# Kernel optimization log

Measured on AMD Instinct MI355X. Metric: run time of the kernel, lower is better.

Reference implementation:

```python
import jax, jax.numpy as jnp
import numpy as np

BLANK = 0
ALPHA = 0.25
GAMMA = 2.0
NEG = -1e30  # log-domain 'minus infinity' (finite to stay autodiff/bf16 safe)


def setup_inputs() -> dict:
    key = jax.random.key(0)
    k1, k2, k3 = jax.random.split(key, 3)
    B, T, C, S = 32, 512, 4000, 40
    tokens_btc = jax.random.normal(k1, (B, T, C), dtype=jnp.float32)
    targets_bxt = jax.random.randint(k2, (B, S), 1, C)            # labels exclude blank=0
    targets_lengths_bx1 = jax.random.randint(k3, (B,), 10, S + 1)  # per-sample target lengths
    return {
        "tokens_btc": tokens_btc,
        "targets_bxt": targets_bxt,
        "targets_lengths_bx1": targets_lengths_bx1,
    }


def _ctc_loss(log_probs_tbc, targets, target_lengths, blank):
    """Log-domain CTC forward (alpha) recursion; input lengths == T for all samples.
    Returns per-sample negative log likelihood, shape [B]."""
    T, B, C = log_probs_tbc.shape
    S = targets.shape[1]
    L = 2 * S + 1  # extended target: blank-interleaved
    ext = jnp.full((B, L), blank, dtype=targets.dtype).at[:, 1::2].set(targets)
    # skip transition (s-2 -> s) allowed iff ext[s] != blank and ext[s] != ext[s-2]
    same_as_2back = jnp.concatenate(
        [jnp.ones((B, 2), bool), ext[:, 2:] == ext[:, :-2]], axis=1)
    skip_ok = (ext != blank) & (~same_as_2back)  # [B, L]

    b_idx = jnp.arange(B)[:, None]
    lp_ext = log_probs_tbc[:, b_idx, ext]  # [T, B, L] gathered emission log-probs

    alpha0 = jnp.full((B, L), NEG, log_probs_tbc.dtype)
    alpha0 = alpha0.at[:, 0].set(lp_ext[0, :, 0]).at[:, 1].set(lp_ext[0, :, 1])

    pad1 = jnp.full((B, 1), NEG, log_probs_tbc.dtype)
    pad2 = jnp.full((B, 2), NEG, log_probs_tbc.dtype)

    def step(alpha, lp_t):
        s1 = jnp.concatenate([pad1, alpha[:, :-1]], axis=1)
        s2 = jnp.concatenate([pad2, alpha[:, :-2]], axis=1)
        a = jnp.logaddexp(alpha, s1)
        a = jnp.where(skip_ok, jnp.logaddexp(a, s2), a)
        return a + lp_t, None

    alphaT, _ = jax.lax.scan(step, alpha0, lp_ext[1:])
    end = 2 * target_lengths  # index of final blank in extended sequence
    a_last = jnp.take_along_axis(alphaT, end[:, None], axis=1)[:, 0]
    a_prev = jnp.take_along_axis(alphaT, (end - 1)[:, None], axis=1)[:, 0]
    loss = -jnp.logaddexp(a_last, a_prev)
    # zero_infinity=True: clamp infinite losses to 0
    return jnp.where(loss < 1e29, loss, 0.0)


def reference(tokens_btc, targets_bxt, targets_lengths_bx1):
    # [B,T,C] -> [T,B,C], log_softmax over classes
    log_probs_tbc = jax.nn.log_softmax(tokens_btc, axis=-1).swapaxes(0, 1)
    loss = _ctc_loss(log_probs_tbc, targets_bxt, targets_lengths_bx1, BLANK)
    # focal reweighting (alpha>0 and gamma>=0 -> enabled)
    pt = jnp.exp(-loss)
    loss = ALPHA * (1.0 - pt) ** GAMMA * loss
    return jnp.mean(loss)
```

## Files before the change

kernel.cpp:

```cpp
#include <hip/hip_runtime.h>


constexpr int B = 32;
constexpr int T = 512;
constexpr int C = 4000;
constexpr int S = 40;
constexpr int L = 2 * S + 1;
constexpr int LPS = 82;
constexpr int PF = 8;

#define NEGV -1e30f

__device__ __forceinline__ float lae(float a, float b) {
    float m = fmaxf(a, b);
    float d = fabsf(a - b);
    return m + __logf(1.0f + __expf(-d));
}

__device__ __forceinline__ float shr1_fill_neg(float x) {
    return __int_as_float(__builtin_amdgcn_update_dpp(
        __float_as_int(NEGV), __float_as_int(x),
        0x138 , 0xF, 0xF, false));
}

__global__ __launch_bounds__(256) void lse_gather_kernel(
        const float* __restrict__ tok,
        const int*   __restrict__ tgt,
        float*       __restrict__ lp) {
    const int wave = threadIdx.x >> 6, lane = threadIdx.x & 63;
    const int row  = blockIdx.x * 4 + wave;
    const int b    = row >> 9;
    const size_t row_off = (size_t)row * C;
    const float4* row4 = (const float4*)(tok + row_off);

    float s = 0.0f;
    #pragma unroll
    for (int k = 0; k < 16; ++k) {
        const int i = lane + 64 * k;
        if (i < C / 4) {
            float4 v = row4[i];
            s += __expf(v.x) + __expf(v.y) + __expf(v.z) + __expf(v.w);
        }
    }
    #pragma unroll
    for (int off = 32; off; off >>= 1) s += __shfl_xor(s, off);
    const float lse = __logf(s);

    float* dst = lp + (size_t)row * LPS;
    {
        const int l = lane;
        int lab = 0;
        if (l & 1) lab = tgt[b * S + (l >> 1)];
        dst[l] = tok[row_off + lab] - lse;
    }
    if (lane < LPS - 64) {
        const int l = 64 + lane;
        float v = 0.0f;
        if (l < L) {
            int lab = 0;
            if (l & 1) lab = tgt[b * S + (l >> 1)];
            v = tok[row_off + lab] - lse;
        }
        dst[l] = v;
    }
}

__global__ __launch_bounds__(64) void ctc_alpha_kernel(
        const float* __restrict__ lp,
        const int*   __restrict__ tgt,
        const int*   __restrict__ lens,
        float*       __restrict__ loss_b)
{
    const int b = blockIdx.x;
    const int lane = threadIdx.x;
    const int ii = (lane < 41) ? lane : 40;

    const float2* base2 = (const float2*)(lp + (size_t)b * T * LPS);

    int ti = tgt[b * S + ((ii < 39) ? ii : 39)];
    int tp = __shfl_up(ti, 1);
    const bool skip1 = (lane >= 1) && (lane <= 39) && (ti != tp);

    float2 v0 = base2[ii];
    float a0 = (lane == 0) ? v0.x : NEGV;
    float a1 = (lane == 0) ? v0.y : NEGV;

    float2 buf[PF];
    #pragma unroll
    for (int k = 0; k < PF; ++k) buf[k] = base2[(size_t)(1 + k) * 41 + ii];

    auto step = [&](float2 v) {
        float p1 = shr1_fill_neg(a1);
        float m0 = fmaxf(a0, p1);
        float n0 = m0 + __logf(__expf(a0 - m0) + __expf(p1 - m0));
        float q  = skip1 ? p1 : NEGV;
        float m1 = fmaxf(fmaxf(a1, a0), q);
        float n1 = m1 + __logf(__expf(a1 - m1) + __expf(a0 - m1) + __expf(q - m1));
        a0 = n0 + v.x;
        a1 = n1 + v.y;
    };

    int t = 1;
    for (; t + (PF - 1) < T; t += PF) {
        #pragma unroll
        for (int k = 0; k < PF; ++k) {
            float2 v = buf[k];
            buf[k] = base2[(size_t)(t + PF + k) * 41 + ii];
            step(v);
        }
    }
    #pragma unroll
    for (int k = 0; k < PF; ++k) {
        if (t + k < T) step(buf[k]);
    }

    const int len = lens[b];
    float ae = __shfl(a0, len);
    float ap = __shfl(a1, len - 1);
    if (lane == 0) {
        float loss = -lae(ae, ap);
        if (!(loss < 1e29f)) loss = 0.0f;
        float pt = __expf(-loss);
        float om = 1.0f - pt;
        loss_b[b] = 0.25f * om * om * loss;
    }
}

__global__ __launch_bounds__(64) void reduce_mean_kernel(
        const float* __restrict__ loss_b, float* __restrict__ out) {
    const int lane = threadIdx.x;
    float v = (lane < B) ? loss_b[lane] : 0.0f;
    #pragma unroll
    for (int off = 32; off; off >>= 1) v += __shfl_down(v, off);
    if (lane == 0) out[0] = v * (1.0f / B);
}

extern "C" void kernel_launch(void* const* d_in, const int* in_sizes, int n_in,
                              void* d_out, int out_size, void* d_ws, size_t ws_size,
                              hipStream_t stream) {
    const float* tok  = (const float*)d_in[0];
    const int*   tgt  = (const int*)d_in[1];
    const int*   lens = (const int*)d_in[2];
    float* out = (float*)d_out;

    float* lp     = (float*)d_ws;
    float* loss_b = lp + (size_t)B * T * LPS + 1024;

    lse_gather_kernel<<<B * T / 4, 256, 0, stream>>>(tok, tgt, lp);
    ctc_alpha_kernel<<<B, 64, 0, stream>>>(lp, tgt, lens, loss_b);
    reduce_mean_kernel<<<1, 64, 0, stream>>>(loss_b, out);
}
```

Baseline: 424.3 us.

## Fuse LSE gather and CTC alpha recursion with per-row flags to overlap stages

Merges the log-softmax gather, the CTC alpha recursion and the mean reduction into one persistent kernel. Gather blocks process rows in time-major order and set a per-row ready flag, while 8 extra blocks run the per-sample alpha recursion, spinning on 8-row flag chunks so the sequential recursion overlaps the bandwidth-bound gather. The final mean is done by the last finishing wave through an atomic counter, which removes two kernel launches. The risk is deadlock if the consumer blocks are resident while gather blocks cannot be scheduled, plus extra cost from flag polling and atomic stores.

After: 407.4 us. -4.0%, faster.

```diff
diff --git a/kernel.cpp b/kernel.cpp
--- a/kernel.cpp
+++ b/kernel.cpp
@@ -7,7 +7,10 @@
 constexpr int S = 40;
 constexpr int L = 2 * S + 1;
 constexpr int LPS = 82;
-constexpr int PF = 8;
+
+constexpr int GATHER_BLOCKS = 1016;
+constexpr int GW = GATHER_BLOCKS * 4;
+constexpr int NBLK = GATHER_BLOCKS + 8;
 
 #define NEGV -1e30f
 
@@ -23,72 +26,83 @@
         0x138 , 0xF, 0xF, false));
 }
 
-__global__ __launch_bounds__(256) void lse_gather_kernel(
+__global__ __launch_bounds__(256) void zero_flags_kernel(unsigned int* p, int n) {
+    const int i = blockIdx.x * 256 + threadIdx.x;
+    if (i < n) p[i] = 0u;
+}
+
+__global__ __launch_bounds__(256, 4) void fused_kernel(
         const float* __restrict__ tok,
         const int*   __restrict__ tgt,
-        float*       __restrict__ lp) {
+        const int*   __restrict__ lens,
+        float*       __restrict__ lp,
+        unsigned char* __restrict__ flags,
+        unsigned int* __restrict__ ctr,
+        float*       __restrict__ loss_b,
+        float*       __restrict__ out) {
     const int wave = threadIdx.x >> 6, lane = threadIdx.x & 63;
-    const int row  = blockIdx.x * 4 + wave;
-    const int b    = row >> 9;
-    const size_t row_off = (size_t)row * C;
-    const float4* row4 = (const float4*)(tok + row_off);
-
-    float s = 0.0f;
-    #pragma unroll
-    for (int k = 0; k < 16; ++k) {
-        const int i = lane + 64 * k;
-        if (i < C / 4) {
-            float4 v = row4[i];
-            s += __expf(v.x) + __expf(v.y) + __expf(v.z) + __expf(v.w);
+
+    if (blockIdx.x < GATHER_BLOCKS) {
+        const int wg = blockIdx.x * 4 + wave;
+        for (int rp = wg; rp < B * T; rp += GW) {
+            const int t  = rp >> 5;
+            const int bb = rp & 31;
+            const int row = (bb << 9) + t;
+            const size_t row_off = (size_t)row * C;
+            const float4* row4 = (const float4*)(tok + row_off);
+
+            float s = 0.0f;
+            #pragma unroll
+            for (int k = 0; k < 16; ++k) {
+                const int i = lane + 64 * k;
+                if (i < C / 4) {
+                    float4 v = row4[i];
+                    s += __expf(v.x) + __expf(v.y) + __expf(v.z) + __expf(v.w);
+                }
+            }
+            #pragma unroll
+            for (int off = 32; off; off >>= 1) s += __shfl_xor(s, off);
+            const float lse = __logf(s);
+
+            float* dst = lp + (size_t)row * LPS;
+            {
+                const int l = lane;
+                int lab = 0;
+                if (l & 1) lab = tgt[bb * S + (l >> 1)];
+                __hip_atomic_store(dst + l, tok[row_off + lab] - lse,
+                                   __ATOMIC_RELAXED, __HIP_MEMORY_SCOPE_AGENT);
+            }
+            if (lane < LPS - 64) {
+                const int l = 64 + lane;
+                float v = 0.0f;
+                if (l < L) {
+                    int lab = 0;
+                    if (l & 1) lab = tgt[bb * S + (l >> 1)];
+                    v = tok[row_off + lab] - lse;
+                }
+                __hip_atomic_store(dst + l, v,
+                                   __ATOMIC_RELAXED, __HIP_MEMORY_SCOPE_AGENT);
+            }
+            asm volatile("s_waitcnt vmcnt(0)" ::: "memory");
+            if (lane == 0)
+                __hip_atomic_store(flags + row, (unsigned char)1,
+                                   __ATOMIC_RELAXED, __HIP_MEMORY_SCOPE_AGENT);
         }
-    }
-    #pragma unroll
-    for (int off = 32; off; off >>= 1) s += __shfl_xor(s, off);
-    const float lse = __logf(s);
-
-    float* dst = lp + (size_t)row * LPS;
-    {
-        const int l = lane;
-        int lab = 0;
-        if (l & 1) lab = tgt[b * S + (l >> 1)];
-        dst[l] = tok[row_off + lab] - lse;
-    }
-    if (lane < LPS - 64) {
-        const int l = 64 + lane;
-        float v = 0.0f;
-        if (l < L) {
-            int lab = 0;
-            if (l & 1) lab = tgt[b * S + (l >> 1)];
-            v = tok[row_off + lab] - lse;
-        }
-        dst[l] = v;
-    }
-}
-
-__global__ __launch_bounds__(64) void ctc_alpha_kernel(
-        const float* __restrict__ lp,
-        const int*   __restrict__ tgt,
-        const int*   __restrict__ lens,
-        float*       __restrict__ loss_b)
-{
-    const int b = blockIdx.x;
-    const int lane = threadIdx.x;
+        return;
+    }
+
+    const int b  = ((blockIdx.x - GATHER_BLOCKS) << 2) + wave;
     const int ii = (lane < 41) ? lane : 40;
-
     const float2* base2 = (const float2*)(lp + (size_t)b * T * LPS);
+    unsigned long long* fw = (unsigned long long*)(flags + ((size_t)b << 9));
+    const unsigned long long ONESW = 0x0101010101010101ull;
 
     int ti = tgt[b * S + ((ii < 39) ? ii : 39)];
     int tp = __shfl_up(ti, 1);
     const bool skip1 = (lane >= 1) && (lane <= 39) && (ti != tp);
-
-    float2 v0 = base2[ii];
-    float a0 = (lane == 0) ? v0.x : NEGV;
-    float a1 = (lane == 0) ? v0.y : NEGV;
-
-    float2 buf[PF];
-    #pragma unroll
-    for (int k = 0; k < PF; ++k) buf[k] = base2[(size_t)(1 + k) * 41 + ii];
-
+    const int len = lens[b];
+
+    float a0, a1;
     auto step = [&](float2 v) {
         float p1 = shr1_fill_neg(a1);
         float m0 = fmaxf(a0, p1);
@@ -100,21 +114,47 @@
         a1 = n1 + v.y;
     };
 
-    int t = 1;
-    for (; t + (PF - 1) < T; t += PF) {
-        #pragma unroll
-        for (int k = 0; k < PF; ++k) {
-            float2 v = buf[k];
-            buf[k] = base2[(size_t)(t + PF + k) * 41 + ii];
-            step(v);
-        }
+    float2 bufA[8], bufB[8];
+    unsigned long long pf = 0;
+
+#define SPINCHUNK(c) do {                                                     \
+        while (pf != ONESW)                                                   \
+            pf = __hip_atomic_load(&fw[(c)], __ATOMIC_RELAXED,                \
+                                   __HIP_MEMORY_SCOPE_AGENT);                 \
+        __builtin_amdgcn_fence(__ATOMIC_ACQUIRE, "agent");                    \
+    } while (0)
+#define PREFETCHF(c) pf = ((c) < 64)                                          \
+        ? __hip_atomic_load(&fw[(c)], __ATOMIC_RELAXED,                       \
+                            __HIP_MEMORY_SCOPE_AGENT)                         \
+        : ONESW
+#define LOADCHUNK(buf, c) do { const int _t0 = (c) << 3;                      \
+        _Pragma("unroll")                                                     \
+        for (int _k = 0; _k < 8; ++_k)                                        \
+            buf[_k] = base2[(size_t)(_t0 + _k) * 41 + ii];                    \
+    } while (0)
+#define STEP8(buf) do { _Pragma("unroll")                                     \
+        for (int _k = 0; _k < 8; ++_k) step(buf[_k]); } while (0)
+
+    SPINCHUNK(0); LOADCHUNK(bufA, 0);
+    pf = 0; SPINCHUNK(1); LOADCHUNK(bufB, 1);
+    PREFETCHF(2);
+
+    {
+        float2 v0 = bufA[0];
+        a0 = (lane == 0) ? v0.x : NEGV;
+        a1 = (lane == 0) ? v0.y : NEGV;
     }
     #pragma unroll
-    for (int k = 0; k < PF; ++k) {
-        if (t + k < T) step(buf[k]);
-    }
-
-    const int len = lens[b];
+    for (int k = 1; k < 8; ++k) step(bufA[k]);
+
+    for (int c = 1; c < 63; c += 2) {
+        SPINCHUNK(c + 1); LOADCHUNK(bufA, c + 1); PREFETCHF(c + 2);
+        STEP8(bufB);
+        SPINCHUNK(c + 2); LOADCHUNK(bufB, c + 2); PREFETCHF(c + 3);
+        STEP8(bufA);
+    }
+    STEP8(bufB);
+
     float ae = __shfl(a0, len);
     float ap = __shfl(a1, len - 1);
     if (lane == 0) {
@@ -122,17 +162,26 @@
         if (!(loss < 1e29f)) loss = 0.0f;
         float pt = __expf(-loss);
         float om = 1.0f - pt;
-        loss_b[b] = 0.25f * om * om * loss;
-    }
-}
-
-__global__ __launch_bounds__(64) void reduce_mean_kernel(
-        const float* __restrict__ loss_b, float* __restrict__ out) {
-    const int lane = threadIdx.x;
-    float v = (lane < B) ? loss_b[lane] : 0.0f;
-    #pragma unroll
-    for (int off = 32; off; off >>= 1) v += __shfl_down(v, off);
-    if (lane == 0) out[0] = v * (1.0f / B);
+        __hip_atomic_store(loss_b + b, 0.25f * om * om * loss,
+                           __ATOMIC_RELAXED, __HIP_MEMORY_SCOPE_AGENT);
+    }
+    asm volatile("s_waitcnt vmcnt(0)" ::: "memory");
+    unsigned int old = 0;
+    if (lane == 0)
+        old = __hip_atomic_fetch_add(ctr, 1u, __ATOMIC_RELAXED,
+                                     __HIP_MEMORY_SCOPE_AGENT);
+    old = (unsigned int)__shfl((int)old, 0);
+    if (old == B - 1) {
+        __builtin_amdgcn_fence(__ATOMIC_ACQUIRE, "agent");
+        float v = (lane < B) ? loss_b[lane] : 0.0f;
+        #pragma unroll
+        for (int off = 32; off; off >>= 1) v += __shfl_down(v, off);
+        if (lane == 0) out[0] = v * (1.0f / B);
+    }
+#undef SPINCHUNK
+#undef PREFETCHF
+#undef LOADCHUNK
+#undef STEP8
 }
 
 extern "C" void kernel_launch(void* const* d_in, const int* in_sizes, int n_in,
@@ -143,10 +192,12 @@
     const int*   lens = (const int*)d_in[2];
     float* out = (float*)d_out;
 
-    float* lp     = (float*)d_ws;
-    float* loss_b = lp + (size_t)B * T * LPS + 1024;
-
-    lse_gather_kernel<<<B * T / 4, 256, 0, stream>>>(tok, tgt, lp);
-    ctc_alpha_kernel<<<B, 64, 0, stream>>>(lp, tgt, lens, loss_b);
-    reduce_mean_kernel<<<1, 64, 0, stream>>>(loss_b, out);
-}
+    float* lp = (float*)d_ws;
+    unsigned char* flags = (unsigned char*)(lp + (size_t)B * T * LPS);
+    unsigned int* ctr = (unsigned int*)(flags + B * T);
+    float* loss_b = (float*)(flags + B * T + 64);
+
+    zero_flags_kernel<<<17, 256, 0, stream>>>((unsigned int*)flags, 4112);
+    fused_kernel<<<NBLK, 256, 0, stream>>>(tok, tgt, lens, lp, flags, ctr,
+                                           loss_b, out);
+}
```
